# Kernel optimization log

Measured on AMD Instinct MI355X. Metric: run time of the kernel, lower is better.

The kernel has to match this reference:

```python
import jax, jax.numpy as jnp
import numpy as np

B, R, C, H = 2048, 100, 64, 256  # batch graphs, regions/graph, in_channels, hidden
N = B * R                         # total nodes
E = 3276800                       # edges


def setup_inputs() -> dict:
    key = jax.random.key(0)
    ks = jax.random.split(key, 12)
    state = jax.random.normal(ks[0], (N, C), dtype=jnp.float32)
    edge_index = jax.random.randint(ks[1], (2, E), 0, N, dtype=jnp.int64)
    action = jax.random.uniform(ks[2], (B, R, R), dtype=jnp.float32)
    s = lambda f: 1.0 / np.sqrt(f)
    W_gcn = jax.random.uniform(ks[3], (C, C), jnp.float32, -s(C), s(C))
    b_gcn = jnp.zeros((C,), jnp.float32)
    W1 = jax.random.uniform(ks[4], (C + R, H), jnp.float32, -s(C + R), s(C + R))
    b1 = jax.random.uniform(ks[5], (H,), jnp.float32, -s(C + R), s(C + R))
    W2 = jax.random.uniform(ks[6], (H, H), jnp.float32, -s(H), s(H))
    b2 = jax.random.uniform(ks[7], (H,), jnp.float32, -s(H), s(H))
    W3 = jax.random.uniform(ks[8], (H, 1), jnp.float32, -s(H), s(H))
    b3 = jax.random.uniform(ks[9], (1,), jnp.float32, -s(H), s(H))
    return {"state": state, "edge_index": edge_index, "action": action,
            "W_gcn": W_gcn, "b_gcn": b_gcn, "W1": W1, "b1": b1,
            "W2": W2, "b2": b2, "W3": W3, "b3": b3}


def gcn_conv(x, edge_index, W, b):
    # PyG GCNConv: add self-loops, symmetric degree normalization, then aggregate.
    n = x.shape[0]
    loops = jnp.arange(n, dtype=edge_index.dtype)
    src = jnp.concatenate([edge_index[0], loops])
    dst = jnp.concatenate([edge_index[1], loops])
    deg = jax.ops.segment_sum(jnp.ones_like(dst, dtype=x.dtype), dst, num_segments=n)
    dinv = deg ** -0.5  # deg >= 1 thanks to self-loops
    xw = x @ W
    msg = xw[src] * (dinv[src] * dinv[dst])[:, None]
    return jax.ops.segment_sum(msg, dst, num_segments=n) + b


def reference(state, edge_index, action, W_gcn, b_gcn, W1, b1, W2, b2, W3, b3):
    out = jax.nn.relu(gcn_conv(state, edge_index, W_gcn, b_gcn))
    x = out + state                              # residual, [N, C]
    x = x.reshape(-1, R, C)                      # [B, R, C]
    concat = jnp.concatenate([x, action], axis=-1)  # [B, R, C+R]
    x = jax.nn.relu(concat @ W1 + b1)
    x = jax.nn.relu(x @ W2 + b2)
    x = jnp.sum(x, axis=1)                       # sum pooling over regions -> [B, H]
    return (x @ W3 + b3).squeeze(-1)             # [B]
```

## Files before the change

kernel.cpp:

```cpp
#include <hip/hip_runtime.h>
#include <hip/hip_bf16.h>
#include <cstdint>
#include <cstddef>

#define N_NODES 204800
#define N_EDGES 3276800
#define NB 2048
#define NR 100
#define NC 64
#define NH 256
#define KPAD 192
#define NBKT 400

typedef __attribute__((ext_vector_type(8))) short short8;
typedef __attribute__((ext_vector_type(4))) float f32x4;
typedef unsigned int uint32;

__device__ __forceinline__ void gload16(const void* g, void* l) {
    __builtin_amdgcn_global_load_lds(
        (const __attribute__((address_space(1))) uint32_t*)(g),
        (__attribute__((address_space(3))) uint32_t*)(l), 16, 0, 0);
}

__device__ __forceinline__ ushort f2bf(float v) {
    __hip_bfloat16 h = __float2bfloat16(v);
    return *reinterpret_cast<ushort*>(&h);
}

__device__ __forceinline__ uint32 pack2bf(float a, float b) {
    return (uint32)f2bf(a) | ((uint32)f2bf(b) << 16);
}

__device__ __forceinline__ float bflo(uint32 v) { return __uint_as_float(v << 16); }
__device__ __forceinline__ float bfhi(uint32 v) { return __uint_as_float(v & 0xFFFF0000u); }


__global__ __launch_bounds__(256) void k_bhist(const int* __restrict__ ei,
                                               int* __restrict__ bcnt) {
    __shared__ int h[NBKT];
    int t = threadIdx.x;
    for (int i = t; i < NBKT; i += 256) h[i] = 0;
    __syncthreads();
    #pragma unroll 8
    for (int k = 0; k < 8; ++k) {
        int e = blockIdx.x * 2048 + k * 256 + t;
        atomicAdd(&h[ei[N_EDGES + e] >> 9], 1);
    }
    __syncthreads();
    for (int i = t; i < NBKT; i += 256)
        if (h[i]) atomicAdd(&bcnt[i], h[i]);
}

__global__ void k_bscan(const int* __restrict__ bcnt, int* __restrict__ boffs,
                        int* __restrict__ bcur) {
    __shared__ int tmp[512];
    int t = threadIdx.x;
    int v = (t < NBKT) ? bcnt[t] : 0;
    tmp[t] = v;
    __syncthreads();
    for (int off = 1; off < 512; off <<= 1) {
        int x = 0;
        if (t >= off) x = tmp[t - off];
        __syncthreads();
        tmp[t] += x;
        __syncthreads();
    }
    if (t < NBKT) {
        int o = tmp[t] - v;
        boffs[t] = o;
        bcur[t] = o;
    }
}

__global__ __launch_bounds__(256) void k_bscat(const int* __restrict__ ei,
                                               int* __restrict__ bcur,
                                               uint32* __restrict__ part) {
    __shared__ int hist[NBKT];
    int tid = threadIdx.x;
    for (int i = tid; i < NBKT; i += 256) hist[i] = 0;
    __syncthreads();

    uint32 w[8];
    int bk[8], r[8];
    #pragma unroll 8
    for (int k = 0; k < 8; ++k) {
        int e = blockIdx.x * 2048 + k * 256 + tid;
        int s = ei[e];
        int d = ei[N_EDGES + e];
        int b = d >> 9;
        w[k] = (uint32)s | ((uint32)(d & 511) << 18);
        bk[k] = b;
        r[k] = atomicAdd(&hist[b], 1);
    }
    __syncthreads();
    for (int i = tid; i < NBKT; i += 256) {
        int c = hist[i];
        hist[i] = c ? atomicAdd(&bcur[i], c) : 0;
    }
    __syncthreads();
    #pragma unroll 8
    for (int k = 0; k < 8; ++k)
        part[hist[bk[k]] + r[k]] = w[k];
}

__global__ __launch_bounds__(512) void k_sortb(
    const uint32* __restrict__ part, const int* __restrict__ boffs,
    const int* __restrict__ bcnt, int* __restrict__ csr,
    int* __restrict__ cnt, int* __restrict__ offs, float* __restrict__ dinv) {
    __shared__ int h[512];
    __shared__ int cur[512];
    int b = blockIdx.x, t = threadIdx.x;
    h[t] = 0;
    __syncthreads();
    int base = boffs[b], n = bcnt[b];
    for (int i = t; i < n; i += 512)
        atomicAdd(&h[part[base + i] >> 18], 1);
    __syncthreads();
    int v = h[t];
    int node = b * 512 + t;
    cnt[node] = v;
    dinv[node] = rsqrtf((float)(v + 1));
    __syncthreads();
    for (int off = 1; off < 512; off <<= 1) {
        int x = 0;
        if (t >= off) x = h[t - off];
        __syncthreads();
        h[t] += x;
        __syncthreads();
    }
    int excl = h[t] - v;
    offs[node] = base + excl;
    cur[t] = excl;
    __syncthreads();
    for (int i = t; i < n; i += 512) {
        uint32 ew = part[base + i];
        int dl = ew >> 18;
        int pos = atomicAdd(&cur[dl], 1);
        csr[base + pos] = (int)(ew & 0x3FFFF);
    }
}

__global__ void k_ssb(const float* __restrict__ state, const float* __restrict__ dinv,
                      uint32* __restrict__ ssb32) {
    int idx = blockIdx.x * 256 + threadIdx.x;
    int row = idx >> 5;
    float d = dinv[row];
    float2 v = reinterpret_cast<const float2*>(state)[idx];
    ssb32[idx] = pack2bf(v.x * d, v.y * d);
}

__global__ __launch_bounds__(256) void k_gcn(
    const uint32* __restrict__ ssb32, const float* __restrict__ state,
    const int* __restrict__ csr, const int* __restrict__ offs,
    const int* __restrict__ cnt, const float* __restrict__ dinv,
    const ushort* __restrict__ Wgt, const float* __restrict__ bg,
    ushort* __restrict__ xb16) {
    __shared__ uint32 av[32 * 36];
    __shared__ ushort wgs[64 * 72];
    int tid = threadIdx.x;
    int w = tid >> 6, lane = tid & 63;
    int half = lane >> 5, l = lane & 31;
    int R0 = blockIdx.x * 32;

    {
        int r = tid >> 2, c0 = (tid & 3) * 16;
        short8 v0 = *(const short8*)(Wgt + r * 64 + c0);
        short8 v1 = *(const short8*)(Wgt + r * 64 + c0 + 8);
        *(short8*)(wgs + r * 72 + c0) = v0;
        *(short8*)(wgs + r * 72 + c0 + 8) = v1;
    }

    for (int rr = 0; rr < 4; ++rr) {
        int lrow = w * 8 + rr * 2 + half;
        int row = R0 + lrow;
        float di = dinv[row];
        float2 st2 = *reinterpret_cast<const float2*>(state + (size_t)row * 64 + 2 * l);
        int s0 = offs[row], c = cnt[row];
        float x0 = 0.f, y0 = 0.f, x1 = 0.f, y1 = 0.f;
        float x2 = 0.f, y2 = 0.f, x3 = 0.f, y3 = 0.f;
        int e = 0;
        for (; e + 8 <= c; e += 8) {
            int sa = csr[s0 + e + 0];
            int sb = csr[s0 + e + 1];
            int sc = csr[s0 + e + 2];
            int sd = csr[s0 + e + 3];
            int se = csr[s0 + e + 4];
            int sf = csr[s0 + e + 5];
            int sg = csr[s0 + e + 6];
            int sh = csr[s0 + e + 7];
            uint32 va = ssb32[(size_t)sa * 32 + l];
            uint32 vb = ssb32[(size_t)sb * 32 + l];
            uint32 vc = ssb32[(size_t)sc * 32 + l];
            uint32 vd = ssb32[(size_t)sd * 32 + l];
            uint32 ve = ssb32[(size_t)se * 32 + l];
            uint32 vf = ssb32[(size_t)sf * 32 + l];
            uint32 vg = ssb32[(size_t)sg * 32 + l];
            uint32 vh = ssb32[(size_t)sh * 32 + l];
            x0 += bflo(va); y0 += bfhi(va);
            x1 += bflo(vb); y1 += bfhi(vb);
            x2 += bflo(vc); y2 += bfhi(vc);
            x3 += bflo(vd); y3 += bfhi(vd);
            x0 += bflo(ve); y0 += bfhi(ve);
            x1 += bflo(vf); y1 += bfhi(vf);
            x2 += bflo(vg); y2 += bfhi(vg);
            x3 += bflo(vh); y3 += bfhi(vh);
        }
        for (; e + 4 <= c; e += 4) {
            int sa = csr[s0 + e + 0];
            int sb = csr[s0 + e + 1];
            int sc = csr[s0 + e + 2];
            int sd = csr[s0 + e + 3];
            uint32 va = ssb32[(size_t)sa * 32 + l];
            uint32 vb = ssb32[(size_t)sb * 32 + l];
            uint32 vc = ssb32[(size_t)sc * 32 + l];
            uint32 vd = ssb32[(size_t)sd * 32 + l];
            x0 += bflo(va); y0 += bfhi(va);
            x1 += bflo(vb); y1 += bfhi(vb);
            x2 += bflo(vc); y2 += bfhi(vc);
            x3 += bflo(vd); y3 += bfhi(vd);
        }
        for (; e < c; ++e) {
            int s = csr[s0 + e];
            uint32 v = ssb32[(size_t)s * 32 + l];
            x0 += bflo(v); y0 += bfhi(v);
        }
        float ax = ((x0 + x1) + (x2 + x3)) * di + di * di * st2.x;
        float ay = ((y0 + y1) + (y2 + y3)) * di + di * di * st2.y;
        av[lrow * 36 + l] = pack2bf(ax, ay);
    }
    __syncthreads();

    int l15 = lane & 15, l4 = lane >> 4;
    const ushort* avs = (const ushort*)av;
    f32x4 acc[2] = {};
    #pragma unroll
    for (int kk = 0; kk < 2; ++kk) {
        short8 bf = *(const short8*)(wgs + (w * 16 + l15) * 72 + kk * 32 + l4 * 8);
        #pragma unroll
        for (int mt = 0; mt < 2; ++mt) {
            short8 af = *(const short8*)(avs + (mt * 16 + l15) * 72 + kk * 32 + l4 * 8);
            acc[mt] = __builtin_amdgcn_mfma_f32_16x16x32_bf16(af, bf, acc[mt], 0, 0, 0);
        }
    }
    int col = w * 16 + l15;
    float bgv = bg[col];
    #pragma unroll
    for (int mt = 0; mt < 2; ++mt)
        #pragma unroll
        for (int r = 0; r < 4; ++r) {
            int row = R0 + mt * 16 + l4 * 4 + r;
            float v = fmaxf(acc[mt][r] + bgv, 0.f) + state[(size_t)row * 64 + col];
            xb16[(size_t)row * 64 + col] = f2bf(v);
        }
}

__global__ void k_packW(const float* __restrict__ W1, const float* __restrict__ W2,
                        const float* __restrict__ Wg, const float* __restrict__ b1,
                        ushort* __restrict__ W1f, ushort* __restrict__ W2f,
                        ushort* __restrict__ Wgt) {
    int t = blockIdx.x * 256 + threadIdx.x;
    if (t < 6 * 4 * 256 * 8) {
        int u = t & 7, chunk = t >> 3;
        int tid = chunk & 255, ktI = chunk >> 8;
        int kt = ktI >> 2, i = ktI & 3;
        int l = tid & 63, wp = tid >> 6;
        int k = kt * 32 + (l >> 4) * 8 + u;
        int j = i * 64 + wp * 16 + (l & 15);
        ushort v = 0;
        if (k < NC + NR) v = f2bf(W1[(size_t)k * NH + j]);
        else if (k == NC + NR) v = f2bf(b1[j]);
        W1f[t] = v;
    } else if (t < 49152 + 8 * 4 * 256 * 8) {
        int t2 = t - 49152;
        int u = t2 & 7, chunk = t2 >> 3;
        int tid = chunk & 255, ktI = chunk >> 8;
        int kt = ktI >> 2, i = ktI & 3;
        int l = tid & 63, wp = tid >> 6;
        int k = kt * 32 + (l >> 4) * 8 + u;
        int j = i * 64 + wp * 16 + (l & 15);
        W2f[t2] = f2bf(W2[(size_t)k * NH + j]);
    } else {
        int t3 = t - 49152 - 65536;
        if (t3 < 64 * 64) {
            int n = t3 >> 6, k = t3 & 63;
            Wgt[t3] = f2bf(Wg[(size_t)k * 64 + n]);
        }
    }
}

__global__ __launch_bounds__(512, 4) void k_mlpf(
    const ushort* __restrict__ xb16, const float* __restrict__ action,
    const ushort* __restrict__ W1f, const ushort* __restrict__ W2f,
    const float* __restrict__ b2, const float* __restrict__ W3,
    float* __restrict__ out) {
    __shared__ __align__(16) ushort Bs[2][256 * 32];
    int tid = threadIdx.x;
    int w = tid >> 6, lane = tid & 63;
    int s = lane & 15, g = lane >> 4;
    int m0 = blockIdx.x * 128;
    int myrow = m0 + w * 16 + s;
    int gb = myrow / 100, grr = myrow - gb * 100;
    const float* abp = action + (size_t)gb * 10000 + (size_t)grr * 100;

    short8 xf0 = *(const short8*)(xb16 + (size_t)myrow * 64 + g * 8);
    short8 xf1 = *(const short8*)(xb16 + (size_t)myrow * 64 + 32 + g * 8);

    #pragma unroll
    for (int tc = 0; tc < 2; ++tc)
        gload16(W1f + ((size_t)(0 * 1024 + tc * 512 + tid)) * 8,
                (char*)Bs[0] + (tc * 512 + tid) * 16);
    __syncthreads();

    f32x4 acc1[16] = {};
    float4 pa0 = {0.f, 0.f, 0.f, 0.f}, pa1 = {0.f, 0.f, 0.f, 0.f};
    int cur = 0;

    #pragma unroll
    for (int kt = 0; kt < 6; ++kt) {
        int nxt = cur ^ 1;
        short8 bf;
        if (kt == 0) bf = xf0;
        else if (kt == 1) bf = xf1;
        else if (kt < 5) {
            ushort tm[8];
            tm[0] = f2bf(pa0.x); tm[1] = f2bf(pa0.y); tm[2] = f2bf(pa0.z); tm[3] = f2bf(pa0.w);
            tm[4] = f2bf(pa1.x); tm[5] = f2bf(pa1.y); tm[6] = f2bf(pa1.z); tm[7] = f2bf(pa1.w);
            bf = *(const short8*)tm;
        } else {
            ushort tm[8];
            if (g == 0) {
                tm[0] = f2bf(pa0.x); tm[1] = f2bf(pa0.y); tm[2] = f2bf(pa0.z); tm[3] = f2bf(pa0.w);
                tm[4] = (ushort)0x3F80; tm[5] = 0; tm[6] = 0; tm[7] = 0;
            } else {
                #pragma unroll
                for (int u = 0; u < 8; ++u) tm[u] = 0;
            }
            bf = *(const short8*)tm;
        }
        if (kt >= 1 && kt <= 3) {
            int c0 = (kt + 1) * 32 - 64 + g * 8;
            pa0 = *(const float4*)(abp + c0);
            pa1 = *(const float4*)(abp + c0 + 4);
        } else if (kt == 4) {
            if (g == 0) pa0 = *(const float4*)(abp + 96);
        }
        if (kt < 5) {
            #pragma unroll
            for (int tc = 0; tc < 2; ++tc)
                gload16(W1f + ((size_t)((kt + 1) * 1024 + tc * 512 + tid)) * 8,
                        (char*)Bs[nxt] + (tc * 512 + tid) * 16);
        } else {
            #pragma unroll
            for (int tc = 0; tc < 2; ++tc)
                gload16(W2f + ((size_t)(0 * 1024 + tc * 512 + tid)) * 8,
                        (char*)Bs[nxt] + (tc * 512 + tid) * 16);
        }
        #pragma unroll
        for (int jt = 0; jt < 16; ++jt) {
            short8 af = *(const short8*)((const char*)Bs[cur] + jt * 1024 + lane * 16);
            acc1[jt] = __builtin_amdgcn_mfma_f32_16x16x32_bf16(af, bf, acc1[jt], 0, 0, 0);
        }
        __syncthreads();
        cur = nxt;
    }

    uint32 q0[16], q1[16];
    #pragma unroll
    for (int jt = 0; jt < 16; ++jt) {
        q0[jt] = pack2bf(fmaxf(acc1[jt][0], 0.f), fmaxf(acc1[jt][1], 0.f));
        q1[jt] = pack2bf(fmaxf(acc1[jt][2], 0.f), fmaxf(acc1[jt][3], 0.f));
    }

    f32x4 acc2[16] = {};
    int src0 = ((lane & 16) << 1) | s;
    int src1 = src0 + 16;
    bool hiSel = (lane & 32) != 0;
    #pragma unroll
    for (int kt = 0; kt < 8; ++kt) {
        int nxt = cur ^ 1;
        if (kt < 7) {
            #pragma unroll
            for (int tc = 0; tc < 2; ++tc)
                gload16(W2f + ((size_t)((kt + 1) * 1024 + tc * 512 + tid)) * 8,
                        (char*)Bs[nxt] + (tc * 512 + tid) * 16);
        }
        uint32 al0 = (uint32)__shfl((int)q0[2 * kt],     src0);
        uint32 ah0 = (uint32)__shfl((int)q0[2 * kt + 1], src0);
        uint32 bl0 = (uint32)__shfl((int)q1[2 * kt],     src0);
        uint32 bh0 = (uint32)__shfl((int)q1[2 * kt + 1], src0);
        uint32 al1 = (uint32)__shfl((int)q0[2 * kt],     src1);
        uint32 ah1 = (uint32)__shfl((int)q0[2 * kt + 1], src1);
        uint32 bl1 = (uint32)__shfl((int)q1[2 * kt],     src1);
        uint32 bh1 = (uint32)__shfl((int)q1[2 * kt + 1], src1);
        short8 af;
        uint32* afp = (uint32*)&af;
        afp[0] = hiSel ? ah0 : al0;
        afp[1] = hiSel ? bh0 : bl0;
        afp[2] = hiSel ? ah1 : al1;
        afp[3] = hiSel ? bh1 : bl1;
        #pragma unroll
        for (int nt = 0; nt < 16; ++nt) {
            short8 bf = *(const short8*)((const char*)Bs[cur] + nt * 1024 + lane * 16);
            acc2[nt] = __builtin_amdgcn_mfma_f32_16x16x32_bf16(af, bf, acc2[nt], 0, 0, 0);
        }
        __syncthreads();
        cur = nxt;
    }

    float vsum[4] = {0.f, 0.f, 0.f, 0.f};
    #pragma unroll
    for (int nt = 0; nt < 16; ++nt) {
        float b2v = b2[nt * 16 + s];
        float w3v = W3[nt * 16 + s];
        #pragma unroll
        for (int r = 0; r < 4; ++r)
            vsum[r] += fmaxf(acc2[nt][r] + b2v, 0.f) * w3v;
    }
    float* red = (float*)Bs;
    #pragma unroll
    for (int r = 0; r < 4; ++r) {
        float v = vsum[r];
        v += __shfl_xor(v, 1);
        v += __shfl_xor(v, 2);
        v += __shfl_xor(v, 4);
        v += __shfl_xor(v, 8);
        if (s == 0) red[w * 16 + g * 4 + r] = v;
    }
    __syncthreads();
    if (tid < 128) {
        float sv = red[tid];
        int half64 = tid >> 6;
        int lt = tid & 63;
        int gbase = m0 + half64 * 64;
        int g0 = gbase / 100;
        int r0 = gbase - g0 * 100;
        int split = 100 - r0; if (split > 64) split = 64;
        float v0 = (lt < split) ? sv : 0.f;
        float vs = sv;
        #pragma unroll
        for (int d = 1; d < 64; d <<= 1) {
            v0 += __shfl_xor(v0, d);
            vs += __shfl_xor(vs, d);
        }
        if (lt == 0) {
            atomicAdd(&out[g0], v0);
            if (split < 64) atomicAdd(&out[g0 + 1], vs - v0);
        }
    }
}

__global__ void k_init_out(float* __restrict__ out, const float* __restrict__ b3) {
    int i = blockIdx.x * 256 + threadIdx.x;
    out[i] = b3[0];
}


extern "C" void kernel_launch(void* const* d_in, const int* in_sizes, int n_in,
                              void* d_out, int out_size, void* d_ws, size_t ws_size,
                              hipStream_t stream) {
    const float* state  = (const float*)d_in[0];
    const int*   ei     = (const int*)d_in[1];
    const float* action = (const float*)d_in[2];
    const float* Wg     = (const float*)d_in[3];
    const float* bg     = (const float*)d_in[4];
    const float* W1     = (const float*)d_in[5];
    const float* b1     = (const float*)d_in[6];
    const float* W2     = (const float*)d_in[7];
    const float* b2     = (const float*)d_in[8];
    const float* W3     = (const float*)d_in[9];
    const float* b3     = (const float*)d_in[10];
    float* out = (float*)d_out;

    char* ws = (char*)d_ws;
    uint32* part  = (uint32*)(ws + 0);
    uint32* ssb32 = (uint32*)(ws + 13107200);
    ushort* xb16  = (ushort*)(ws + 39321600);
    int*   csr    = (int*)  (ws + 65536000);
    int*   cnt    = (int*)  (ws + 78643200);
    int*   offs   = (int*)  (ws + 79462400);
    float* dinv   = (float*)(ws + 80281600);
    int*   bcnt   = (int*)  (ws + 81100800);
    int*   boffs  = (int*)  (ws + 81102400);
    int*   bcur   = (int*)  (ws + 81104000);
    ushort* W1f   = (ushort*)(ws + 81105600);
    ushort* W2f   = (ushort*)(ws + 81203904);
    ushort* Wgt   = (ushort*)(ws + 81334976);

    hipMemsetAsync(bcnt, 0, NBKT * sizeof(int), stream);
    k_init_out<<<NB / 256, 256, 0, stream>>>(out, b3);

    k_bhist<<<N_EDGES / 2048, 256, 0, stream>>>(ei, bcnt);
    k_bscan<<<1, 512, 0, stream>>>(bcnt, boffs, bcur);
    k_bscat<<<N_EDGES / 2048, 256, 0, stream>>>(ei, bcur, part);
    k_sortb<<<NBKT, 512, 0, stream>>>(part, boffs, bcnt, csr, cnt, offs, dinv);
    k_ssb<<<(N_NODES * 32) / 256, 256, 0, stream>>>(state, dinv, ssb32);
    k_packW<<<(49152 + 65536 + 4096 + 255) / 256, 256, 0, stream>>>(
        W1, W2, Wg, b1, W1f, W2f, Wgt);
    k_gcn<<<N_NODES / 32, 256, 0, stream>>>(ssb32, state, csr, offs, cnt, dinv,
                                            Wgt, bg, xb16);
    k_mlpf<<<N_NODES / 128, 512, 0, stream>>>(xb16, action, W1f, W2f, b2, W3, out);
}
```

Baseline: 302.1 us.

## Fuse state scaling into bucket sort and double edges per block in histogram/scatter

The edge histogram and scatter kernels now handle 4096 edges per block instead of 2048, halving the block count. The scatter kernel is restructured into two passes: a histogram pass, then a pass that re-reads the edges and places each one via a shared-memory atomic cursor, instead of keeping per-edge ranks in registers. The separate kernel that scales state by dinv and packs it to bf16 is folded into the end of the per-bucket sort kernel, using dinv kept in shared memory. This removes one launch and the dinv reload, at the cost of reading the destination indices twice in the scatter and adding serial work at the tail of the 400-block sort kernel.

```diff
diff --git a/kernel.cpp b/kernel.cpp
--- a/kernel.cpp
+++ b/kernel.cpp
@@ -41,9 +41,9 @@
     int t = threadIdx.x;
     for (int i = t; i < NBKT; i += 256) h[i] = 0;
     __syncthreads();
-    #pragma unroll 8
-    for (int k = 0; k < 8; ++k) {
-        int e = blockIdx.x * 2048 + k * 256 + t;
+    #pragma unroll 16
+    for (int k = 0; k < 16; ++k) {
+        int e = blockIdx.x * 4096 + k * 256 + t;
         atomicAdd(&h[ei[N_EDGES + e] >> 9], 1);
     }
     __syncthreads();
@@ -76,39 +76,40 @@
                                                int* __restrict__ bcur,
                                                uint32* __restrict__ part) {
     __shared__ int hist[NBKT];
+    __shared__ int curb[NBKT];
     int tid = threadIdx.x;
     for (int i = tid; i < NBKT; i += 256) hist[i] = 0;
     __syncthreads();
-
-    uint32 w[8];
-    int bk[8], r[8];
-    #pragma unroll 8
-    for (int k = 0; k < 8; ++k) {
-        int e = blockIdx.x * 2048 + k * 256 + tid;
+    #pragma unroll 16
+    for (int k = 0; k < 16; ++k) {
+        int e = blockIdx.x * 4096 + k * 256 + tid;
+        atomicAdd(&hist[ei[N_EDGES + e] >> 9], 1);
+    }
+    __syncthreads();
+    for (int i = tid; i < NBKT; i += 256) {
+        int c = hist[i];
+        curb[i] = c ? atomicAdd(&bcur[i], c) : 0;
+    }
+    __syncthreads();
+    #pragma unroll 16
+    for (int k = 0; k < 16; ++k) {
+        int e = blockIdx.x * 4096 + k * 256 + tid;
         int s = ei[e];
         int d = ei[N_EDGES + e];
         int b = d >> 9;
-        w[k] = (uint32)s | ((uint32)(d & 511) << 18);
-        bk[k] = b;
-        r[k] = atomicAdd(&hist[b], 1);
-    }
-    __syncthreads();
-    for (int i = tid; i < NBKT; i += 256) {
-        int c = hist[i];
-        hist[i] = c ? atomicAdd(&bcur[i], c) : 0;
-    }
-    __syncthreads();
-    #pragma unroll 8
-    for (int k = 0; k < 8; ++k)
-        part[hist[bk[k]] + r[k]] = w[k];
+        int p = atomicAdd(&curb[b], 1);
+        part[p] = (uint32)s | ((uint32)(d & 511) << 18);
+    }
 }
 
 __global__ __launch_bounds__(512) void k_sortb(
     const uint32* __restrict__ part, const int* __restrict__ boffs,
     const int* __restrict__ bcnt, int* __restrict__ csr,
-    int* __restrict__ cnt, int* __restrict__ offs, float* __restrict__ dinv) {
+    int* __restrict__ cnt, int* __restrict__ offs, float* __restrict__ dinv,
+    const float* __restrict__ state, uint32* __restrict__ ssb32) {
     __shared__ int h[512];
     __shared__ int cur[512];
+    __shared__ float sdv[512];
     int b = blockIdx.x, t = threadIdx.x;
     h[t] = 0;
     __syncthreads();
@@ -119,7 +120,9 @@
     int v = h[t];
     int node = b * 512 + t;
     cnt[node] = v;
-    dinv[node] = rsqrtf((float)(v + 1));
+    float dv = rsqrtf((float)(v + 1));
+    dinv[node] = dv;
+    sdv[t] = dv;
     __syncthreads();
     for (int off = 1; off < 512; off <<= 1) {
         int x = 0;
@@ -138,15 +141,14 @@
         int pos = atomicAdd(&cur[dl], 1);
         csr[base + pos] = (int)(ew & 0x3FFFF);
     }
-}
-
-__global__ void k_ssb(const float* __restrict__ state, const float* __restrict__ dinv,
-                      uint32* __restrict__ ssb32) {
-    int idx = blockIdx.x * 256 + threadIdx.x;
-    int row = idx >> 5;
-    float d = dinv[row];
-    float2 v = reinterpret_cast<const float2*>(state)[idx];
-    ssb32[idx] = pack2bf(v.x * d, v.y * d);
+    __syncthreads();
+    for (int i = t; i < 512 * 32; i += 512) {
+        int nl = i >> 5, u = i & 31;
+        float d = sdv[nl];
+        size_t idx = (size_t)(b * 512 + nl) * 32 + u;
+        float2 sv = reinterpret_cast<const float2*>(state)[idx];
+        ssb32[idx] = pack2bf(sv.x * d, sv.y * d);
+    }
 }
 
 __global__ __launch_bounds__(256) void k_gcn(
@@ -489,11 +491,11 @@
     hipMemsetAsync(bcnt, 0, NBKT * sizeof(int), stream);
     k_init_out<<<NB / 256, 256, 0, stream>>>(out, b3);
 
-    k_bhist<<<N_EDGES / 2048, 256, 0, stream>>>(ei, bcnt);
+    k_bhist<<<N_EDGES / 4096, 256, 0, stream>>>(ei, bcnt);
     k_bscan<<<1, 512, 0, stream>>>(bcnt, boffs, bcur);
-    k_bscat<<<N_EDGES / 2048, 256, 0, stream>>>(ei, bcur, part);
-    k_sortb<<<NBKT, 512, 0, stream>>>(part, boffs, bcnt, csr, cnt, offs, dinv);
-    k_ssb<<<(N_NODES * 32) / 256, 256, 0, stream>>>(state, dinv, ssb32);
+    k_bscat<<<N_EDGES / 4096, 256, 0, stream>>>(ei, bcur, part);
+    k_sortb<<<NBKT, 512, 0, stream>>>(part, boffs, bcnt, csr, cnt, offs, dinv,
+                                      state, ssb32);
     k_packW<<<(49152 + 65536 + 4096 + 255) / 256, 256, 0, stream>>>(
         W1, W2, Wg, b1, W1f, W2f, Wgt);
     k_gcn<<<N_NODES / 32, 256, 0, stream>>>(ssb32, state, csr, offs, cnt, dinv,
```

Measured after the change: 271.0 us (median of 2 runs). 1.12x faster.
